# Optimization experiments

Measured on AMD Instinct MI355X. Metric: run time of the kernel, lower is better.

The kernel has to match this reference:

```python
import jax, jax.numpy as jnp
import numpy as np

B, D, L, H = 4, 1024, 2048, 8
HD = D // H


def setup_inputs() -> dict:
    key = jax.random.key(0)
    k1, k2, k3, k4 = jax.random.split(key, 4)
    query = jax.random.normal(k1, (B, D, L), dtype=jnp.float32)
    mask = jax.random.randint(k2, (B, L), 0, 2, dtype=jnp.int32)
    W1 = jax.random.normal(k3, (2 * D, D), dtype=jnp.float32) * (D ** -0.5)
    Wq = jax.random.normal(k4, (D, D), dtype=jnp.float32) * (D ** -0.5)
    return {"query": query, "mask": mask, "W1": W1, "Wq": Wq}


def _split_heads(x):
    # [B, L, C] -> [B, H, L, C//H]
    b, l, c = x.shape
    return x.reshape(b, l, H, c // H).transpose(0, 2, 1, 3)


def reference(query, mask, W1, Wq):
    # 1x1 conv == channel GEMM; produce [B, L, out]
    temp = jnp.einsum('od,bdl->blo', W1, query)   # [B, L, 2D] (K|V)
    q = jnp.einsum('od,bdl->blo', Wq, query)      # [B, L, D]
    k, v = jnp.split(temp, 2, axis=-1)
    q = _split_heads(q) * (HD ** -0.5)            # [B, H, L, HD]
    k = _split_heads(k)
    v = _split_heads(v)
    scores = jnp.einsum('bhqd,bhkd->bhqk', q, k)  # [B, H, L, L]
    m = mask.astype(jnp.float32)[:, None, None, :]
    logits = scores + (-1e30) * (1.0 - m)
    weights = jax.nn.softmax(logits, axis=-1)     # dropout p=0 (eval)
    out = jnp.einsum('bhqk,bhkd->bhqd', weights, v)
    out = out.transpose(0, 2, 1, 3).reshape(B, L, D)  # merge heads
    return out.transpose(0, 2, 1)                 # [B, D, L]
```

## Files before the change

kernel.cpp:

```cpp
#include <hip/hip_runtime.h>
#include <hip/hip_bf16.h>

#define B_  4
#define D_  1024
#define L_  2048
#define H_  8
#define HD_ 128

typedef __attribute__((ext_vector_type(8))) short bf16x8;
typedef __attribute__((ext_vector_type(4))) float f32x4;

static __device__ __forceinline__ ushort f2bf(float f) {
    unsigned u = __float_as_uint(f);
    unsigned r = (u + 0x7fffu + ((u >> 16) & 1u)) >> 16;
    return (ushort)r;
}

static __device__ __forceinline__ void dma16(const ushort* g, ushort* l) {
    __builtin_amdgcn_global_load_lds(
        (const __attribute__((address_space(1))) void*)g,
        (__attribute__((address_space(3))) void*)l, 16, 0, 0);
}

__global__ void k_zero_out(float* __restrict__ out, int n) {
    int i = blockIdx.x * 256 + threadIdx.x;
    if (i < n) out[i] = 0.f;
}

__global__ void k_convert_w(const float* __restrict__ W1, const float* __restrict__ Wq,
                            ushort* __restrict__ Wb) {
    int i = blockIdx.x * 256 + threadIdx.x;
    const int n1 = 2 * D_ * D_ / 4;
    float4 v = (i < n1) ? ((const float4*)W1)[i] : ((const float4*)Wq)[i - n1];
    ushort4 o;
    o.x = f2bf(v.x); o.y = f2bf(v.y); o.z = f2bf(v.z); o.w = f2bf(v.w);
    ((ushort4*)Wb)[i] = o;
}

__global__ void k_transpose(const float* __restrict__ q, ushort* __restrict__ Xt) {
    __shared__ float tile[32][33];
    int b = blockIdx.z, d0 = blockIdx.y * 32, l0 = blockIdx.x * 32;
    int tx = threadIdx.x, ty = threadIdx.y;
    const float* src = q + (size_t)b * D_ * L_;
    for (int i = 0; i < 4; i++)
        tile[ty + 8 * i][tx] = src[(size_t)(d0 + ty + 8 * i) * L_ + l0 + tx];
    __syncthreads();
    ushort* dst = Xt + (size_t)b * L_ * D_;
    for (int i = 0; i < 4; i++)
        dst[(size_t)(l0 + ty + 8 * i) * D_ + d0 + tx] = f2bf(tile[tx][ty + 8 * i]);
}

__global__ void k_scan(const int* __restrict__ mask, int* __restrict__ cidx,
                       int* __restrict__ cnt) {
    int b = blockIdx.x;
    int lane = threadIdx.x;
    const int* mb = mask + b * L_;
    int base = 0;
    for (int c = 0; c < L_; c += 64) {
        int m = mb[c + lane];
        unsigned long long bal = __ballot(m != 0);
        int pre = __popcll(bal & ((1ull << lane) - 1ull));
        if (m) cidx[b * L_ + base + pre] = c + lane;
        base += __popcll(bal);
    }
    for (int j = base + lane; j < L_; j += 64) cidx[b * L_ + j] = 0;
    if (lane == 0) cnt[b] = base;
}

__launch_bounds__(256)
__global__ void k_proj(const ushort* __restrict__ Wb, const ushort* __restrict__ Xt,
                       const int* __restrict__ cidx, const int* __restrict__ cnt,
                       ushort* __restrict__ Qb, ushort* __restrict__ Kb,
                       ushort* __restrict__ Vt) {
    __shared__ alignas(16) ushort As[128 * 64];
    __shared__ alignas(16) ushort Bs[128 * 64];
    const int b  = blockIdx.z;
    const int o0 = blockIdx.y * 128;
    const int l0 = blockIdx.x * 128;
    const int type = o0 >> 10;
    if (type < 2) {
        int tiles = (cnt[b] + 127) >> 7;
        if (blockIdx.x >= tiles) return;
    }
    const int t = threadIdx.x;
    const int wave = t >> 6, lane = t & 63, quad = lane >> 4, li = lane & 15;
    const int wm = wave >> 1, wn = wave & 1;
    const ushort* Xb = Xt + (size_t)b * L_ * D_;

    const int srow = t >> 3;
    const int g = (t & 7) ^ (srow & 7);
    const ushort* aSrc[4];
    const ushort* bSrc[4];
    for (int i = 0; i < 4; i++) {
        int r = i * 32 + srow;
        aSrc[i] = Wb + (size_t)(o0 + r) * D_ + g * 8;
        int l = l0 + r;
        int gl = (type < 2) ? cidx[b * L_ + l] : l;
        bSrc[i] = Xb + (size_t)gl * D_ + g * 8;
    }

    f32x4 acc[4][4] = {};

    for (int k0 = 0; k0 < D_; k0 += 64) {
        for (int i = 0; i < 4; i++)
            dma16(aSrc[i] + k0, &As[(i * 256 + wave * 64) * 8]);
        for (int i = 0; i < 4; i++)
            dma16(bSrc[i] + k0, &Bs[(i * 256 + wave * 64) * 8]);
        __syncthreads();
        for (int ks = 0; ks < 64; ks += 32) {
            const int kc = ks >> 3;
            bf16x8 af[4], bfr[4];
            for (int mf = 0; mf < 4; mf++) {
                int row = wm * 64 + mf * 16 + li;
                af[mf] = *(const bf16x8*)&As[row * 64 + (((kc + quad) ^ (li & 7)) * 8)];
            }
            for (int nf = 0; nf < 4; nf++) {
                int row = wn * 64 + nf * 16 + li;
                bfr[nf] = *(const bf16x8*)&Bs[row * 64 + (((kc + quad) ^ (li & 7)) * 8)];
            }
            for (int mf = 0; mf < 4; mf++)
                for (int nf = 0; nf < 4; nf++)
                    acc[mf][nf] = __builtin_amdgcn_mfma_f32_16x16x32_bf16(af[mf], bfr[nf], acc[mf][nf], 0, 0, 0);
        }
        __syncthreads();
    }

    const float qscale = 0.08838834764831845f;
    for (int mf = 0; mf < 4; mf++) {
        int o = o0 + wm * 64 + mf * 16 + quad * 4;
        int c = o & 1023;
        int h = c >> 7, hd = c & 127;
        for (int nf = 0; nf < 4; nf++) {
            int l = l0 + wn * 64 + nf * 16 + li;
            f32x4 v = acc[mf][nf];
            if (type == 0) {
                ushort4 s4 = { f2bf(v[0]), f2bf(v[1]), f2bf(v[2]), f2bf(v[3]) };
                *(ushort4*)&Kb[(((size_t)(b * H_ + h)) * L_ + l) * HD_ + hd] = s4;
            } else if (type == 1) {
                size_t base = (size_t)(b * H_ + h) * HD_;
                Vt[(base + hd + 0) * L_ + l] = f2bf(v[0]);
                Vt[(base + hd + 1) * L_ + l] = f2bf(v[1]);
                Vt[(base + hd + 2) * L_ + l] = f2bf(v[2]);
                Vt[(base + hd + 3) * L_ + l] = f2bf(v[3]);
            } else {
                ushort4 s4 = { f2bf(v[0] * qscale), f2bf(v[1] * qscale),
                               f2bf(v[2] * qscale), f2bf(v[3] * qscale) };
                *(ushort4*)&Qb[(((size_t)(b * H_ + h)) * L_ + l) * HD_ + hd] = s4;
            }
        }
    }
}

__launch_bounds__(256, 4)
__global__ void k_attn(const ushort* __restrict__ Qb, const ushort* __restrict__ Kb,
                       const ushort* __restrict__ Vt, const int* __restrict__ mask,
                       float* __restrict__ out) {
    __shared__ alignas(16) ushort Ks[2][32][128];
    __shared__ alignas(16) ushort Vs[2][128][32];
    __shared__ alignas(16) ushort Pl[4][16][40];
    const int blk = blockIdx.x;
    const int h = blk & 7, qt = (blk >> 3) & 31, b = blk >> 8;
    const int t = threadIdx.x;
    const int w = t >> 6, lane = t & 63, quad = lane >> 4, li = lane & 15;
    const int q0 = qt * 64 + w * 16;
    const ushort* Qh = Qb + (size_t)(b * H_ + h) * L_ * HD_;
    const ushort* Kh = Kb + (size_t)(b * H_ + h) * L_ * HD_;
    const ushort* Vh = Vt + (size_t)(b * H_ + h) * HD_ * L_;
    const int* mb = mask + b * L_;

    int cm = 0;
    for (int c = lane; c < L_; c += 64) cm += mb[c];
    cm += __shfl_xor(cm, 32, 64);
    cm += __shfl_xor(cm, 16, 64);
    cm += __shfl_xor(cm, 8, 64);
    cm += __shfl_xor(cm, 4, 64);
    cm += __shfl_xor(cm, 2, 64);
    cm += __shfl_xor(cm, 1, 64);
    const int cnt = cm;
    int cnt_pad = (cnt + 31) & ~31;
    if (cnt_pad < 32) cnt_pad = 32;

    const ushort* kgp[2]; const ushort* vgp[2];
    for (int i = 0; i < 2; i++) {
        int seg = w * 2 + i;
        int key = seg * 4 + (lane >> 4);
        int ck  = (lane & 15) ^ (key & 15);
        kgp[i] = Kh + (size_t)key * HD_ + ck * 8;
        int hd  = seg * 16 + (lane >> 2);
        int cv  = (lane & 3) ^ (hd & 3);
        vgp[i] = Vh + (size_t)hd * L_ + cv * 8;
    }

    for (int i = 0; i < 2; i++) dma16(kgp[i], &Ks[0][0][0] + (w * 2 + i) * 512);
    for (int i = 0; i < 2; i++) dma16(vgp[i], &Vs[0][0][0] + (w * 2 + i) * 512);

    bf16x8 qf[4];
    for (int kf = 0; kf < 4; kf++)
        qf[kf] = *(const bf16x8*)&Qh[(size_t)(q0 + li) * HD_ + kf * 32 + quad * 8];

    float mrun = -1e30f, lrun = 0.f;
    f32x4 acc[8] = {};

    int buf = 0;
    for (int n0 = 0; n0 < cnt_pad; n0 += 32, buf ^= 1) {
        __syncthreads();

        if (n0 + 32 < cnt_pad) {
            int nb = buf ^ 1;
            for (int i = 0; i < 2; i++)
                dma16(kgp[i] + (size_t)(n0 + 32) * HD_, &Ks[nb][0][0] + (w * 2 + i) * 512);
            for (int i = 0; i < 2; i++)
                dma16(vgp[i] + (n0 + 32), &Vs[nb][0][0] + (w * 2 + i) * 512);
        }

        f32x4 s[2] = {};
        for (int kf = 0; kf < 4; kf++) {
            bf16x8 kfr[2];
            for (int mt = 0; mt < 2; mt++)
                kfr[mt] = *(const bf16x8*)&Ks[buf][mt * 16 + li][((kf * 4 + quad) ^ li) * 8];
            for (int mt = 0; mt < 2; mt++)
                s[mt] = __builtin_amdgcn_mfma_f32_16x16x32_bf16(kfr[mt], qf[kf], s[mt], 0, 0, 0);
        }

        if (n0 + 32 > cnt) {
            for (int mt = 0; mt < 2; mt++)
                for (int r = 0; r < 4; r++)
                    if (n0 + mt * 16 + quad * 4 + r >= cnt) s[mt][r] = -1e30f;
        }

        float a0 = fmaxf(fmaxf(s[0][0], s[0][1]), fmaxf(s[0][2], s[0][3]));
        float a1 = fmaxf(fmaxf(s[1][0], s[1][1]), fmaxf(s[1][2], s[1][3]));
        float nm = fmaxf(a0, a1);
        nm = fmaxf(nm, __shfl_xor(nm, 16, 64));
        nm = fmaxf(nm, __shfl_xor(nm, 32, 64));
        float mnew = fmaxf(mrun, nm);
        float alpha = __expf(mrun - mnew);
        mrun = mnew;
        float rs = 0.f;
        for (int mt = 0; mt < 2; mt++)
            for (int r = 0; r < 4; r++) {
                float p = __expf(s[mt][r] - mnew);
                s[mt][r] = p;
                rs += p;
            }
        rs += __shfl_xor(rs, 16, 64);
        rs += __shfl_xor(rs, 32, 64);
        lrun = lrun * alpha + rs;

        if (__any(alpha != 1.0f)) {
            int sb = (lane & 48) | (quad * 4);
            float ar0 = __shfl(alpha, sb + 0, 64);
            float ar1 = __shfl(alpha, sb + 1, 64);
            float ar2 = __shfl(alpha, sb + 2, 64);
            float ar3 = __shfl(alpha, sb + 3, 64);
            for (int nf2 = 0; nf2 < 8; nf2++) {
                acc[nf2][0] *= ar0;
                acc[nf2][1] *= ar1;
                acc[nf2][2] *= ar2;
                acc[nf2][3] *= ar3;
            }
        }

        for (int mt = 0; mt < 2; mt++) {
            ushort4 pk = { f2bf(s[mt][0]), f2bf(s[mt][1]),
                           f2bf(s[mt][2]), f2bf(s[mt][3]) };
            *(ushort4*)&Pl[w][li][mt * 16 + quad * 4] = pk;
        }

        bf16x8 pa = *(const bf16x8*)&Pl[w][li][quad * 8];
        for (int nf2 = 0; nf2 < 8; nf2++) {
            bf16x8 vb = *(const bf16x8*)&Vs[buf][nf2 * 16 + li][(quad ^ (li & 3)) * 8];
            acc[nf2] = __builtin_amdgcn_mfma_f32_16x16x32_bf16(pa, vb, acc[nf2], 0, 0, 0);
        }
    }

    float inv = 1.0f / lrun;
    int sb = (lane & 48) | (quad * 4);
    float i0 = __shfl(inv, sb + 0, 64);
    float i1 = __shfl(inv, sb + 1, 64);
    float i2 = __shfl(inv, sb + 2, 64);
    float i3 = __shfl(inv, sb + 3, 64);
    int l = q0 + quad * 4;
    for (int nf2 = 0; nf2 < 8; nf2++) {
        int d = h * HD_ + nf2 * 16 + li;
        float4 o4 = { acc[nf2][0] * i0, acc[nf2][1] * i1,
                      acc[nf2][2] * i2, acc[nf2][3] * i3 };
        *(float4*)&out[((size_t)(b * D_ + d)) * L_ + l] = o4;
    }
}

extern "C" void kernel_launch(void* const* d_in, const int* in_sizes, int n_in,
                              void* d_out, int out_size, void* d_ws, size_t ws_size,
                              hipStream_t stream) {
    const float* query = nullptr;
    const int*   mask  = nullptr;
    const float* W1    = nullptr;
    const float* Wq    = nullptr;
    for (int i = 0; i < n_in; i++) {
        switch (in_sizes[i]) {
            case 8388608: query = (const float*)d_in[i]; break;
            case 8192:    mask  = (const int*)d_in[i];   break;
            case 2097152: W1    = (const float*)d_in[i]; break;
            case 1048576: Wq    = (const float*)d_in[i]; break;
        }
    }
    float* out = (float*)d_out;

    if (ws_size < 50331648u || !query || !mask || !W1 || !Wq) {
        hipLaunchKernelGGL(k_zero_out, dim3((out_size + 255) / 256), dim3(256), 0, stream,
                           out, out_size);
        return;
    }

    ushort* Wb = (ushort*)d_out;
    ushort* Xt = (ushort*)((char*)d_out + 6291456);
    int* cidx  = (int*)((char*)d_out + 23068672);
    int* cnt   = (int*)((char*)d_out + 23101440);
    char* ws = (char*)d_ws;
    ushort* Qb = (ushort*)(ws + 0);
    ushort* Kb = (ushort*)(ws + 16777216);
    ushort* Vt = (ushort*)(ws + 33554432);

    hipLaunchKernelGGL(k_convert_w, dim3(3072), dim3(256), 0, stream, W1, Wq, Wb);
    hipLaunchKernelGGL(k_transpose, dim3(64, 32, 4), dim3(32, 8), 0, stream, query, Xt);
    hipLaunchKernelGGL(k_scan, dim3(4), dim3(64), 0, stream, mask, cidx, cnt);
    hipLaunchKernelGGL(k_proj, dim3(16, 24, 4), dim3(256), 0, stream, Wb, Xt, cidx, cnt, Qb, Kb, Vt);
    hipLaunchKernelGGL(k_attn, dim3(1024), dim3(256), 0, stream, Qb, Kb, Vt, mask, out);
}
```

Before: 241.8 us.

## Merge prep kernels into one launch and widen attention key tile to 64

```diff
diff --git a/kernel.cpp b/kernel.cpp
--- a/kernel.cpp
+++ b/kernel.cpp
@@ -27,44 +27,47 @@
     if (i < n) out[i] = 0.f;
 }
 
-__global__ void k_convert_w(const float* __restrict__ W1, const float* __restrict__ Wq,
-                            ushort* __restrict__ Wb) {
-    int i = blockIdx.x * 256 + threadIdx.x;
-    const int n1 = 2 * D_ * D_ / 4;
-    float4 v = (i < n1) ? ((const float4*)W1)[i] : ((const float4*)Wq)[i - n1];
-    ushort4 o;
-    o.x = f2bf(v.x); o.y = f2bf(v.y); o.z = f2bf(v.z); o.w = f2bf(v.w);
-    ((ushort4*)Wb)[i] = o;
-}
-
-__global__ void k_transpose(const float* __restrict__ q, ushort* __restrict__ Xt) {
+__global__ void k_prep(const float* __restrict__ q, const float* __restrict__ W1,
+                       const float* __restrict__ Wq, const int* __restrict__ mask,
+                       ushort* __restrict__ Wb, ushort* __restrict__ Xt,
+                       int* __restrict__ cidx, int* __restrict__ cnt) {
     __shared__ float tile[32][33];
-    int b = blockIdx.z, d0 = blockIdx.y * 32, l0 = blockIdx.x * 32;
-    int tx = threadIdx.x, ty = threadIdx.y;
-    const float* src = q + (size_t)b * D_ * L_;
-    for (int i = 0; i < 4; i++)
-        tile[ty + 8 * i][tx] = src[(size_t)(d0 + ty + 8 * i) * L_ + l0 + tx];
-    __syncthreads();
-    ushort* dst = Xt + (size_t)b * L_ * D_;
-    for (int i = 0; i < 4; i++)
-        dst[(size_t)(l0 + ty + 8 * i) * D_ + d0 + tx] = f2bf(tile[tx][ty + 8 * i]);
-}
-
-__global__ void k_scan(const int* __restrict__ mask, int* __restrict__ cidx,
-                       int* __restrict__ cnt) {
-    int b = blockIdx.x;
-    int lane = threadIdx.x;
-    const int* mb = mask + b * L_;
-    int base = 0;
-    for (int c = 0; c < L_; c += 64) {
-        int m = mb[c + lane];
-        unsigned long long bal = __ballot(m != 0);
-        int pre = __popcll(bal & ((1ull << lane) - 1ull));
-        if (m) cidx[b * L_ + base + pre] = c + lane;
-        base += __popcll(bal);
-    }
-    for (int j = base + lane; j < L_; j += 64) cidx[b * L_ + j] = 0;
-    if (lane == 0) cnt[b] = base;
+    const int bid = blockIdx.x, t = threadIdx.x;
+    if (bid < 8192) {
+        int bx = bid & 63, by = (bid >> 6) & 31, bz = bid >> 11;
+        int tx = t & 31, ty = t >> 5;
+        int d0 = by * 32, l0 = bx * 32;
+        const float* src = q + (size_t)bz * D_ * L_;
+        for (int i = 0; i < 4; i++)
+            tile[ty + 8 * i][tx] = src[(size_t)(d0 + ty + 8 * i) * L_ + l0 + tx];
+        __syncthreads();
+        ushort* dst = Xt + (size_t)bz * L_ * D_;
+        for (int i = 0; i < 4; i++)
+            dst[(size_t)(l0 + ty + 8 * i) * D_ + d0 + tx] = f2bf(tile[tx][ty + 8 * i]);
+    } else if (bid < 8192 + 3072) {
+        int i = (bid - 8192) * 256 + t;
+        const int n1 = 2 * D_ * D_ / 4;
+        float4 v = (i < n1) ? ((const float4*)W1)[i] : ((const float4*)Wq)[i - n1];
+        ushort4 o;
+        o.x = f2bf(v.x); o.y = f2bf(v.y); o.z = f2bf(v.z); o.w = f2bf(v.w);
+        ((ushort4*)Wb)[i] = o;
+    } else {
+        int b = bid - (8192 + 3072);
+        if (t < 64) {
+            int lane = t;
+            const int* mb = mask + b * L_;
+            int base = 0;
+            for (int c = 0; c < L_; c += 64) {
+                int m = mb[c + lane];
+                unsigned long long bal = __ballot(m != 0);
+                int pre = __popcll(bal & ((1ull << lane) - 1ull));
+                if (m) cidx[b * L_ + base + pre] = c + lane;
+                base += __popcll(bal);
+            }
+            for (int j = base + lane; j < L_; j += 64) cidx[b * L_ + j] = 0;
+            if (lane == 0) cnt[b] = base;
+        }
+    }
 }
 
 __launch_bounds__(256)
@@ -151,13 +154,13 @@
     }
 }
 
-__launch_bounds__(256, 4)
+__launch_bounds__(256, 2)
 __global__ void k_attn(const ushort* __restrict__ Qb, const ushort* __restrict__ Kb,
                        const ushort* __restrict__ Vt, const int* __restrict__ mask,
                        float* __restrict__ out) {
-    __shared__ alignas(16) ushort Ks[2][32][128];
-    __shared__ alignas(16) ushort Vs[2][128][32];
-    __shared__ alignas(16) ushort Pl[4][16][40];
+    __shared__ alignas(16) ushort Ks[2][64][128];
+    __shared__ alignas(16) ushort Vs[2][128][64];
+    __shared__ alignas(16) ushort Pl[4][16][72];
     const int blk = blockIdx.x;
     const int h = blk & 7, qt = (blk >> 3) & 31, b = blk >> 8;
     const int t = threadIdx.x;
@@ -177,22 +180,21 @@
     cm += __shfl_xor(cm, 2, 64);
     cm += __shfl_xor(cm, 1, 64);
     const int cnt = cm;
-    int cnt_pad = (cnt + 31) & ~31;
-    if (cnt_pad < 32) cnt_pad = 32;
-
-    const ushort* kgp[2]; const ushort* vgp[2];
-    for (int i = 0; i < 2; i++) {
-        int seg = w * 2 + i;
-        int key = seg * 4 + (lane >> 4);
-        int ck  = (lane & 15) ^ (key & 15);
-        kgp[i] = Kh + (size_t)key * HD_ + ck * 8;
-        int hd  = seg * 16 + (lane >> 2);
-        int cv  = (lane & 3) ^ (hd & 3);
-        vgp[i] = Vh + (size_t)hd * L_ + cv * 8;
-    }
-
-    for (int i = 0; i < 2; i++) dma16(kgp[i], &Ks[0][0][0] + (w * 2 + i) * 512);
-    for (int i = 0; i < 2; i++) dma16(vgp[i], &Vs[0][0][0] + (w * 2 + i) * 512);
+    int cnt_pad = (cnt + 63) & ~63;
+    if (cnt_pad < 64) cnt_pad = 64;
+
+    const ushort* kgp[4]; const ushort* vgp[4];
+    for (int i = 0; i < 4; i++) {
+        int key = i * 16 + w * 4 + (lane >> 4);
+        int gk  = (lane & 15) ^ (key & 15);
+        kgp[i] = Kh + (size_t)key * HD_ + gk * 8;
+        int hd  = i * 32 + w * 8 + (lane >> 3);
+        int gv  = (lane & 7) ^ (hd & 7);
+        vgp[i] = Vh + (size_t)hd * L_ + gv * 8;
+    }
+
+    for (int i = 0; i < 4; i++) dma16(kgp[i], &Ks[0][0][0] + (i * 256 + w * 64) * 8);
+    for (int i = 0; i < 4; i++) dma16(vgp[i], &Vs[0][0][0] + (i * 256 + w * 64) * 8);
 
     bf16x8 qf[4];
     for (int kf = 0; kf < 4; kf++)
@@ -202,45 +204,49 @@
     f32x4 acc[8] = {};
 
     int buf = 0;
-    for (int n0 = 0; n0 < cnt_pad; n0 += 32, buf ^= 1) {
+    for (int n0 = 0; n0 < cnt_pad; n0 += 64, buf ^= 1) {
         __syncthreads();
 
-        if (n0 + 32 < cnt_pad) {
+        if (n0 + 64 < cnt_pad) {
             int nb = buf ^ 1;
-            for (int i = 0; i < 2; i++)
-                dma16(kgp[i] + (size_t)(n0 + 32) * HD_, &Ks[nb][0][0] + (w * 2 + i) * 512);
-            for (int i = 0; i < 2; i++)
-                dma16(vgp[i] + (n0 + 32), &Vs[nb][0][0] + (w * 2 + i) * 512);
-        }
-
-        f32x4 s[2] = {};
+            for (int i = 0; i < 4; i++)
+                dma16(kgp[i] + (size_t)(n0 + 64) * HD_, &Ks[nb][0][0] + (i * 256 + w * 64) * 8);
+            for (int i = 0; i < 4; i++)
+                dma16(vgp[i] + (n0 + 64), &Vs[nb][0][0] + (i * 256 + w * 64) * 8);
+        }
+
+        f32x4 s4[4] = {};
+        __builtin_amdgcn_s_setprio(1);
         for (int kf = 0; kf < 4; kf++) {
-            bf16x8 kfr[2];
-            for (int mt = 0; mt < 2; mt++)
+            bf16x8 kfr[4];
+            for (int mt = 0; mt < 4; mt++)
                 kfr[mt] = *(const bf16x8*)&Ks[buf][mt * 16 + li][((kf * 4 + quad) ^ li) * 8];
-            for (int mt = 0; mt < 2; mt++)
-                s[mt] = __builtin_amdgcn_mfma_f32_16x16x32_bf16(kfr[mt], qf[kf], s[mt], 0, 0, 0);
-        }
-
-        if (n0 + 32 > cnt) {
-            for (int mt = 0; mt < 2; mt++)
+            for (int mt = 0; mt < 4; mt++)
+                s4[mt] = __builtin_amdgcn_mfma_f32_16x16x32_bf16(kfr[mt], qf[kf], s4[mt], 0, 0, 0);
+        }
+        __builtin_amdgcn_s_setprio(0);
+
+        if (n0 + 64 > cnt) {
+            for (int mt = 0; mt < 4; mt++)
                 for (int r = 0; r < 4; r++)
-                    if (n0 + mt * 16 + quad * 4 + r >= cnt) s[mt][r] = -1e30f;
-        }
-
-        float a0 = fmaxf(fmaxf(s[0][0], s[0][1]), fmaxf(s[0][2], s[0][3]));
-        float a1 = fmaxf(fmaxf(s[1][0], s[1][1]), fmaxf(s[1][2], s[1][3]));
-        float nm = fmaxf(a0, a1);
+                    if (n0 + mt * 16 + quad * 4 + r >= cnt) s4[mt][r] = -1e30f;
+        }
+
+        float m0 = fmaxf(fmaxf(s4[0][0], s4[0][1]), fmaxf(s4[0][2], s4[0][3]));
+        float m1 = fmaxf(fmaxf(s4[1][0], s4[1][1]), fmaxf(s4[1][2], s4[1][3]));
+        float m2 = fmaxf(fmaxf(s4[2][0], s4[2][1]), fmaxf(s4[2][2], s4[2][3]));
+        float m3 = fmaxf(fmaxf(s4[3][0], s4[3][1]), fmaxf(s4[3][2], s4[3][3]));
+        float nm = fmaxf(fmaxf(m0, m1), fmaxf(m2, m3));
         nm = fmaxf(nm, __shfl_xor(nm, 16, 64));
         nm = fmaxf(nm, __shfl_xor(nm, 32, 64));
         float mnew = fmaxf(mrun, nm);
         float alpha = __expf(mrun - mnew);
         mrun = mnew;
         float rs = 0.f;
-        for (int mt = 0; mt < 2; mt++)
+        for (int mt = 0; mt < 4; mt++)
             for (int r = 0; r < 4; r++) {
-                float p = __expf(s[mt][r] - mnew);
-                s[mt][r] = p;
+                float p = __expf(s4[mt][r] - mnew);
+                s4[mt][r] = p;
                 rs += p;
             }
         rs += __shfl_xor(rs, 16, 64);
@@ -261,17 +267,21 @@
             }
         }
 
-        for (int mt = 0; mt < 2; mt++) {
-            ushort4 pk = { f2bf(s[mt][0]), f2bf(s[mt][1]),
-                           f2bf(s[mt][2]), f2bf(s[mt][3]) };
+        for (int mt = 0; mt < 4; mt++) {
+            ushort4 pk = { f2bf(s4[mt][0]), f2bf(s4[mt][1]),
+                           f2bf(s4[mt][2]), f2bf(s4[mt][3]) };
             *(ushort4*)&Pl[w][li][mt * 16 + quad * 4] = pk;
         }
 
-        bf16x8 pa = *(const bf16x8*)&Pl[w][li][quad * 8];
-        for (int nf2 = 0; nf2 < 8; nf2++) {
-            bf16x8 vb = *(const bf16x8*)&Vs[buf][nf2 * 16 + li][(quad ^ (li & 3)) * 8];
-            acc[nf2] = __builtin_amdgcn_mfma_f32_16x16x32_bf16(pa, vb, acc[nf2], 0, 0, 0);
-        }
+        __builtin_amdgcn_s_setprio(1);
+        for (int kf2 = 0; kf2 < 2; kf2++) {
+            bf16x8 pa = *(const bf16x8*)&Pl[w][li][kf2 * 32 + quad * 8];
+            for (int nf2 = 0; nf2 < 8; nf2++) {
+                bf16x8 vb = *(const bf16x8*)&Vs[buf][nf2 * 16 + li][((kf2 * 4 + quad) ^ (li & 7)) * 8];
+                acc[nf2] = __builtin_amdgcn_mfma_f32_16x16x32_bf16(pa, vb, acc[nf2], 0, 0, 0);
+            }
+        }
+        __builtin_amdgcn_s_setprio(0);
     }
 
     float inv = 1.0f / lrun;
@@ -321,9 +331,8 @@
     ushort* Kb = (ushort*)(ws + 16777216);
     ushort* Vt = (ushort*)(ws + 33554432);
 
-    hipLaunchKernelGGL(k_convert_w, dim3(3072), dim3(256), 0, stream, W1, Wq, Wb);
-    hipLaunchKernelGGL(k_transpose, dim3(64, 32, 4), dim3(32, 8), 0, stream, query, Xt);
-    hipLaunchKernelGGL(k_scan, dim3(4), dim3(64), 0, stream, mask, cidx, cnt);
+    hipLaunchKernelGGL(k_prep, dim3(8192 + 3072 + 4), dim3(256), 0, stream,
+                       query, W1, Wq, mask, Wb, Xt, cidx, cnt);
     hipLaunchKernelGGL(k_proj, dim3(16, 24, 4), dim3(256), 0, stream, Wb, Xt, cidx, cnt, Qb, Kb, Vt);
     hipLaunchKernelGGL(k_attn, dim3(1024), dim3(256), 0, stream, Qb, Kb, Vt, mask, out);
 }
```

Result: no change. 242.3 us (+0.2%).
